# Performance work log

Measured on AMD Instinct MI355X. Metric: run time of the kernel, lower is better.

## Reference

```python
import jax, jax.numpy as jnp
import numpy as np
from jax import lax

V, E, H, D = 50000, 300, 128, 128   # vocab, embed, gru_units, dense_units
B, S, W, T = 32, 512, 20, 16        # batch, sentences/doc, words/sentence, topics/doc


def setup_inputs() -> dict:
    key = jax.random.key(0)
    ks = jax.random.split(key, 16)
    word_ids = jax.random.randint(ks[0], (B, S, W), 0, V, dtype=jnp.int32)
    # contiguous equal topic segments, 1-based inclusive boundaries
    L = S // T
    starts = (1 + np.arange(T) * L).astype(np.int32)
    ends = (starts + L - 1).astype(np.int32)
    topic_start_ends = jnp.asarray(np.broadcast_to(np.stack([starts, ends], -1), (B, T, 2)))
    sc = 0.05
    def rn(k, shape, s=sc):
        return jax.random.normal(k, shape, dtype=jnp.float32) * s
    inp = {
        "word_ids": word_ids,
        "topic_start_ends": topic_start_ends,
        "emb": rn(ks[1], (V, E), 0.6),
        "Wih_f": rn(ks[2], (3 * H, E)), "Whh_f": rn(ks[3], (3 * H, H)),
        "bih_f": rn(ks[4], (3 * H,)),   "bhh_f": rn(ks[5], (3 * H,)),
        "Wih_b": rn(ks[6], (3 * H, E)), "Whh_b": rn(ks[7], (3 * H, H)),
        "bih_b": rn(ks[8], (3 * H,)),   "bhh_b": rn(ks[9], (3 * H,)),
        "W_att": rn(ks[10], (4 * H, 4 * H)), "v_att": rn(ks[11], (4 * H, 1)),
        "W1": rn(ks[12], (D, 4 * H)), "b1": rn(ks[13], (D,)),
        "W2": rn(ks[14], (1, D)),     "b2": rn(ks[15], (1,)),
    }
    return inp


def _gru_dir(x_sbe, Wih, Whh, bih, bhh, reverse):
    """x_sbe: [S,B,E] -> (outputs [S,B,H] in original time order, last hidden [B,H])."""
    h0 = jnp.zeros((x_sbe.shape[1], Whh.shape[1]), x_sbe.dtype)
    def step(h, xt):
        gx = xt @ Wih.T + bih            # [B,3H]
        gh = h @ Whh.T + bhh
        xr, xz, xn = jnp.split(gx, 3, axis=-1)   # PyTorch gate order: r,z,n
        hr, hz, hn = jnp.split(gh, 3, axis=-1)
        r = jax.nn.sigmoid(xr + hr)
        z = jax.nn.sigmoid(xz + hz)
        n = jnp.tanh(xn + r * hn)
        h2 = (1.0 - z) * n + z * h
        return h2, h2
    last, outs = lax.scan(step, h0, x_sbe, reverse=reverse)
    return outs, last


def reference(word_ids, topic_start_ends, emb,
              Wih_f, Whh_f, bih_f, bhh_f,
              Wih_b, Whh_b, bih_b, bhh_b,
              W_att, v_att, W1, b1, W2, b2):
    # --- sent_encoder: mean word embedding per sentence ---
    x = jnp.mean(emb[word_ids], axis=2)              # [B,S,E]
    # --- doc_encoder: biGRU over sentences ---
    xs = jnp.swapaxes(x, 0, 1)                       # [S,B,E]
    out_f, last_f = _gru_dir(xs, Wih_f, Whh_f, bih_f, bhh_f, reverse=False)
    out_b, last_b = _gru_dir(xs, Wih_b, Whh_b, bih_b, bhh_b, reverse=True)
    sent_rep = jnp.swapaxes(jnp.concatenate([out_f, out_b], axis=-1), 0, 1)  # [B,S,2H]
    # faithful to torch hidden.view(B, 2H) on [2,B,H] contiguous memory
    doc_vec = jnp.stack([last_f, last_b], axis=0).reshape(sent_rep.shape[0], 2 * last_f.shape[1])
    doc_rep = jnp.broadcast_to(doc_vec[:, None, :], sent_rep.shape)          # [B,S,2H]
    # --- topic segment extraction via boundary diffs on zero-padded GRU out ---
    Bn, Sn, twoH = sent_rep.shape
    Hn = twoH // 2
    P = jnp.pad(sent_rep, ((0, 0), (1, 1), (0, 0)))   # [B,S+2,2H]; index i = 1-based sentence i
    starts = topic_start_ends[..., 0]                 # [B,T], 1-based
    ends = topic_start_ends[..., 1]
    bidx = jnp.arange(Bn)[:, None]
    fw = P[bidx, ends, :Hn] - P[bidx, starts - 1, :Hn]      # forward-dir diff
    bw = P[bidx, starts, Hn:] - P[bidx, ends + 1, Hn:]      # backward-dir diff
    topic_mat = jnp.concatenate([fw, bw], axis=-1)          # [B,T,2H]
    # scatter: sentence s (0-based) belongs to topic with starts-1 <= s <= ends-1
    pos = jnp.arange(Sn, dtype=starts.dtype) + 1            # 1-based sentence ids
    seg = jax.vmap(lambda st: jnp.searchsorted(st, pos, side='right') - 1)(starts)  # [B,S]
    topic_rep = jnp.take_along_axis(topic_mat, seg[..., None], axis=1)              # [B,S,2H]
    # --- decoder ---
    cat_ds = jnp.concatenate([doc_rep, sent_rep], axis=-1)   # [B,S,4H]
    cat_ts = jnp.concatenate([topic_rep, sent_rep], axis=-1)
    doc_scores = jnp.tanh(cat_ds @ W_att) @ v_att            # [B,S,1]
    topic_scores = jnp.tanh(cat_ts @ W_att) @ v_att
    ssum = doc_scores + topic_scores
    context = (doc_scores / ssum) * doc_rep + (topic_scores / ssum) * topic_rep
    inp = jnp.concatenate([sent_rep, context], axis=-1)      # [B,S,4H]
    h = jax.nn.relu(inp @ W1.T + b1)                         # dropout = identity (eval)
    logits = h @ W2.T + b2                                   # [B,S,1]
    return logits
```

## Files before the change

kernel.cpp:

```cpp
#include <hip/hip_runtime.h>
#include <hip/hip_bf16.h>

#define B_ 32
#define S_ 512
#define W_ 20
#define T_ 16
#define E_ 300
#define H_ 128
#define M_ (B_*S_)

#define OFF_GX        0ul
#define OFF_X         12582912ul
#define OFF_SENT      17498112ul
#define OFF_LASTF     21692416ul
#define OFF_LASTB     21696512ul
#define OFF_DOCVEC    21700608ul
#define OFF_TOPICMAT  21708800ul
#define OFF_DOCPART   21839872ul
#define OFF_TOPICPART 21856256ul
#define OFF_SEG       22118400ul
#define OFF_WTIH      22134784ul
#define OFF_BIASIH    22365184ul
#define OFF_W1T       22365952ul
#define OFF_H         22431488ul
#define OFF_SRPART    0ul
#define OFF_CTX       OFF_X

__global__ void prep_kernel(const float* __restrict__ Wih_f, const float* __restrict__ Wih_b,
                            const float* __restrict__ bih_f, const float* __restrict__ bih_b,
                            const float* __restrict__ W1,
                            float* __restrict__ Wt_ih, float* __restrict__ bias_ih,
                            float* __restrict__ W1t) {
  int idx = blockIdx.x * 256 + threadIdx.x;
  if (idx < E_ * 768) {
    int k = idx / 768, g = idx % 768;
    Wt_ih[idx] = (g < 384) ? Wih_f[g * E_ + k] : Wih_b[(g - 384) * E_ + k];
  }
  if (idx < 768) bias_ih[idx] = (idx < 384) ? bih_f[idx] : bih_b[idx - 384];
  if (idx < 512 * 128) { int k = idx / 128, j = idx % 128; W1t[idx] = W1[j * 512 + k]; }
}

__global__ void embed_mean_kernel(const int* __restrict__ wid, const float* __restrict__ emb,
                                  float* __restrict__ x) {
  int m = blockIdx.x;
  const int* ids = wid + (size_t)m * W_;
  int e = threadIdx.x;
  float s0 = 0.f, s1 = 0.f, s2 = 0.f;
  for (int w = 0; w < W_; w++) {
    const float* row = emb + (size_t)ids[w] * E_;
    s0 += row[e];
    s1 += row[e + 128];
    if (e < E_ - 256) s2 += row[e + 256];
  }
  const float inv = 1.0f / (float)W_;
  float* xr = x + (size_t)m * E_;
  xr[e] = s0 * inv; xr[e + 128] = s1 * inv; if (e < E_ - 256) xr[e + 256] = s2 * inv;
}

template<bool BIAS, bool ACCUM, bool RELU>
__global__ __launch_bounds__(256) void gemm64(
    const float* __restrict__ A, int lda,
    const float* __restrict__ B, int ldb,
    float* __restrict__ C, int ldc,
    const float* __restrict__ bias,
    int M, int N, int K) {
  __shared__ float As[16][68];
  __shared__ float Bs[16][68];
  const int tid = threadIdx.x;
  const int n0 = blockIdx.x * 64, m0 = blockIdx.y * 64;
  const int tx = tid & 15, ty = tid >> 4;
  const int am = tid >> 2, ak = (tid & 3) << 2;
  const int bk = tid >> 4, bn = (tid & 15) << 2;
  float acc[4][4] = {};
  for (int k0 = 0; k0 < K; k0 += 16) {
    float4 av = make_float4(0.f, 0.f, 0.f, 0.f);
    int arow = m0 + am;
    if (arow < M) {
      if (k0 + ak + 3 < K) {
        av = *(const float4*)(A + (size_t)arow * lda + k0 + ak);
      } else {
        float tmp[4] = {0.f, 0.f, 0.f, 0.f};
        #pragma unroll
        for (int i2 = 0; i2 < 4; i2++) { int k = k0 + ak + i2; if (k < K) tmp[i2] = A[(size_t)arow * lda + k]; }
        av = make_float4(tmp[0], tmp[1], tmp[2], tmp[3]);
      }
    }
    As[ak + 0][am] = av.x; As[ak + 1][am] = av.y; As[ak + 2][am] = av.z; As[ak + 3][am] = av.w;
    float4 bv = make_float4(0.f, 0.f, 0.f, 0.f);
    {
      int k = k0 + bk;
      if (k < K) bv = *(const float4*)(B + (size_t)k * ldb + n0 + bn);
    }
    *(float4*)&Bs[bk][bn] = bv;
    __syncthreads();
    #pragma unroll
    for (int kk = 0; kk < 16; kk++) {
      float4 a = *(const float4*)&As[kk][ty << 2];
      float4 b = *(const float4*)&Bs[kk][tx << 2];
      acc[0][0] = fmaf(a.x, b.x, acc[0][0]); acc[0][1] = fmaf(a.x, b.y, acc[0][1]);
      acc[0][2] = fmaf(a.x, b.z, acc[0][2]); acc[0][3] = fmaf(a.x, b.w, acc[0][3]);
      acc[1][0] = fmaf(a.y, b.x, acc[1][0]); acc[1][1] = fmaf(a.y, b.y, acc[1][1]);
      acc[1][2] = fmaf(a.y, b.z, acc[1][2]); acc[1][3] = fmaf(a.y, b.w, acc[1][3]);
      acc[2][0] = fmaf(a.z, b.x, acc[2][0]); acc[2][1] = fmaf(a.z, b.y, acc[2][1]);
      acc[2][2] = fmaf(a.z, b.z, acc[2][2]); acc[2][3] = fmaf(a.z, b.w, acc[2][3]);
      acc[3][0] = fmaf(a.w, b.x, acc[3][0]); acc[3][1] = fmaf(a.w, b.y, acc[3][1]);
      acc[3][2] = fmaf(a.w, b.z, acc[3][2]); acc[3][3] = fmaf(a.w, b.w, acc[3][3]);
    }
    __syncthreads();
  }
  float4 bias4 = make_float4(0.f, 0.f, 0.f, 0.f);
  if (BIAS) bias4 = *(const float4*)(bias + n0 + (tx << 2));
  #pragma unroll
  for (int i = 0; i < 4; i++) {
    int row = m0 + (ty << 2) + i;
    if (row >= M) break;
    float* cp = C + (size_t)row * ldc + n0 + (tx << 2);
    float4 v = make_float4(acc[i][0], acc[i][1], acc[i][2], acc[i][3]);
    if (BIAS) { v.x += bias4.x; v.y += bias4.y; v.z += bias4.z; v.w += bias4.w; }
    if (ACCUM) { float4 o = *(const float4*)cp; v.x += o.x; v.y += o.y; v.z += o.z; v.w += o.w; }
    if (RELU) { v.x = fmaxf(v.x, 0.f); v.y = fmaxf(v.y, 0.f); v.z = fmaxf(v.z, 0.f); v.w = fmaxf(v.w, 0.f); }
    *(float4*)cp = v;
  }
}

#define PIN4(v) asm volatile("" : "+v"((v).x), "+v"((v).y), "+v"((v).z), "+v"((v).w))
__global__ __launch_bounds__(512) __attribute__((amdgpu_waves_per_eu(2, 2)))
void gru_kernel(
    const float* __restrict__ gxbuf,
    const float* __restrict__ Whh_f, const float* __restrict__ Whh_b,
    const float* __restrict__ bhh_f, const float* __restrict__ bhh_b,
    float* __restrict__ sent_rep,
    float* __restrict__ last_f, float* __restrict__ last_b) {
  const int bid = blockIdx.x;
  const int dir = bid >> 5, b = bid & 31;
  const int t = threadIdx.x;
  const int wave = t >> 6;
  const int lane = t & 63;
  const int q = lane >> 4;
  const int j = (wave << 4) + (lane & 15);
  const int k0 = q << 5;
  const float* Whh = dir ? Whh_b : Whh_f;
  const float* bhh = dir ? bhh_b : bhh_f;

  float4 wr4[8], wz4[8], wn4[8];
  #pragma unroll
  for (int i = 0; i < 8; i++) {
    wr4[i] = *(const float4*)(Whh + (size_t)j * 128 + k0 + i * 4);
    wz4[i] = *(const float4*)(Whh + (size_t)(128 + j) * 128 + k0 + i * 4);
    wn4[i] = *(const float4*)(Whh + (size_t)(256 + j) * 128 + k0 + i * 4);
  }
  #pragma unroll
  for (int i = 0; i < 8; i++) { PIN4(wr4[i]); PIN4(wz4[i]); PIN4(wn4[i]); }

  const float bhr = bhh[j], bhz = bhh[128 + j], bhn = bhh[256 + j];
  const int gate = q ? (q - 1) : 2;
  const float mr = (q == 1) ? 1.f : 0.f;
  const float mz = (q == 2) ? 1.f : 0.f;
  const float* gxp = gxbuf + (size_t)b * 512 * 768 + dir * 384 + gate * 128 + j;

  __shared__ float hbuf[2][128];
  if (t < 128) hbuf[0][t] = 0.f;
  __syncthreads();

  float hprev = 0.f;
  int ts = dir ? 511 : 0;
  const int stp = dir ? -1 : 1;
  float* srow = sent_rep + (size_t)b * 512 * 256 + dir * 128;

  float gx_c = gxp[(size_t)ts * 768];
  float gx_1 = gxp[(size_t)(ts + stp) * 768];

  #pragma unroll 1
  for (int s = 0; s < 512; s++) {
    float gx_2 = 0.f;
    if (s + 2 < 512) gx_2 = gxp[(size_t)(ts + 2 * stp) * 768];
    const float4* h4 = (const float4*)(&hbuf[s & 1][k0]);
    float pr = 0.f, pz = 0.f, pn = 0.f;
    #pragma unroll
    for (int i = 0; i < 8; i++) {
      float4 hv = h4[i];
      pr = fmaf(wr4[i].x, hv.x, pr); pr = fmaf(wr4[i].y, hv.y, pr);
      pr = fmaf(wr4[i].z, hv.z, pr); pr = fmaf(wr4[i].w, hv.w, pr);
      pz = fmaf(wz4[i].x, hv.x, pz); pz = fmaf(wz4[i].y, hv.y, pz);
      pz = fmaf(wz4[i].z, hv.z, pz); pz = fmaf(wz4[i].w, hv.w, pz);
      pn = fmaf(wn4[i].x, hv.x, pn); pn = fmaf(wn4[i].y, hv.y, pn);
      pn = fmaf(wn4[i].z, hv.z, pn); pn = fmaf(wn4[i].w, hv.w, pn);
    }
    pr = fmaf(mr, gx_c, pr);
    pz = fmaf(mz, gx_c, pz);
    pr += __shfl_xor(pr, 16); pr += __shfl_xor(pr, 32);
    pz += __shfl_xor(pz, 16); pz += __shfl_xor(pz, 32);
    pn += __shfl_xor(pn, 16); pn += __shfl_xor(pn, 32);
    float gn = __shfl(gx_c, (lane & 15) + 48);
    float r = 1.f / (1.f + expf(-(pr + bhr)));
    float z = 1.f / (1.f + expf(-(pz + bhz)));
    float n = tanhf(gn + r * (pn + bhn));
    float hnew = (1.f - z) * n + z * hprev;
    hprev = hnew;
    if (q == 0) {
      hbuf[(s + 1) & 1][j] = hnew;
      srow[(size_t)ts * 256 + j] = hnew;
    }
    __syncthreads();
    ts += stp;
    gx_c = gx_1; gx_1 = gx_2;
  }
  if (q == 0) (dir ? last_b : last_f)[b * 128 + j] = hprev;
}

__global__ void docvec_kernel(const float* __restrict__ last_f, const float* __restrict__ last_b,
                              float* __restrict__ doc_vec) {
  int idx = blockIdx.x * 256 + threadIdx.x;
  int i = idx >> 8, c = idx & 255;
  const float* src = (i < 16) ? last_f : last_b;
  int ii = (i < 16) ? i : i - 16;
  int bb = 2 * ii + (c >> 7);
  doc_vec[idx] = src[bb * 128 + (c & 127)];
}

__global__ void topicmat_kernel(const float* __restrict__ sent_rep, const int* __restrict__ tse,
                                float* __restrict__ topic_mat) {
  int bt = blockIdx.x;
  int b = bt >> 4, t = bt & 15;
  int st = tse[(b * 16 + t) * 2 + 0];
  int en = tse[(b * 16 + t) * 2 + 1];
  int jj = threadIdx.x;
  const float* sr = sent_rep + (size_t)b * 512 * 256;
  float val;
  if (jj < 128) {
    float a = sr[(size_t)(en - 1) * 256 + jj];
    float c = (st - 2 >= 0) ? sr[(size_t)(st - 2) * 256 + jj] : 0.f;
    val = a - c;
  } else {
    float a = sr[(size_t)(st - 1) * 256 + jj];
    float c = (en <= 511) ? sr[(size_t)en * 256 + jj] : 0.f;
    val = a - c;
  }
  topic_mat[(size_t)bt * 256 + jj] = val;
}

__global__ void seg_kernel(const int* __restrict__ tse, int* __restrict__ seg) {
  int idx = blockIdx.x * 256 + threadIdx.x;
  int b = idx >> 9, s = idx & 511;
  int pos = s + 1, cnt = 0;
  for (int t = 0; t < T_; t++) cnt += (tse[(b * T_ + t) * 2] <= pos);
  int sg = cnt - 1; sg = sg < 0 ? 0 : (sg > T_ - 1 ? T_ - 1 : sg);
  seg[idx] = sg;
}

__global__ void scores_ctx_kernel(const float* __restrict__ sr_part,
                                  const float* __restrict__ doc_part,
                                  const float* __restrict__ topic_part,
                                  const float* __restrict__ v_att,
                                  const float* __restrict__ doc_vec,
                                  const float* __restrict__ topic_mat,
                                  const int* __restrict__ seg,
                                  float* __restrict__ context) {
  int wid = threadIdx.x >> 6, lane = threadIdx.x & 63;
  int row = blockIdx.x * 4 + wid;
  int b = row >> 9;
  int sg = seg[row];
  const float* srp = sr_part + (size_t)row * 512;
  const float* dp = doc_part + (size_t)b * 512;
  const float* tp = topic_part + (size_t)(b * 16 + sg) * 512;
  float accd = 0.f, acct = 0.f;
  #pragma unroll
  for (int i = 0; i < 8; i++) {
    int n = lane + i * 64;
    float sp = srp[n], va = v_att[n];
    accd += tanhf(dp[n] + sp) * va;
    acct += tanhf(tp[n] + sp) * va;
  }
  #pragma unroll
  for (int off = 32; off; off >>= 1) { accd += __shfl_xor(accd, off); acct += __shfl_xor(acct, off); }
  float ssum = accd + acct;
  float rd = accd / ssum, rt = acct / ssum;
  const float* dv = doc_vec + (size_t)b * 256;
  const float* tm = topic_mat + (size_t)(b * 16 + sg) * 256;
  float* ctx = context + (size_t)row * 256;
  #pragma unroll
  for (int i = 0; i < 4; i++) {
    int jj = lane + i * 64;
    ctx[jj] = rd * dv[jj] + rt * tm[jj];
  }
}

__global__ void logits_kernel(const float* __restrict__ h, const float* __restrict__ W2,
                              const float* __restrict__ b2, float* __restrict__ out, int M) {
  int wid = threadIdx.x >> 6, lane = threadIdx.x & 63;
  int row = blockIdx.x * 4 + wid;
  if (row >= M) return;
  const float* hp = h + (size_t)row * 128;
  float s = hp[lane] * W2[lane] + hp[lane + 64] * W2[lane + 64];
  #pragma unroll
  for (int off = 32; off; off >>= 1) s += __shfl_xor(s, off);
  if (lane == 0) out[row] = s + b2[0];
}

extern "C" void kernel_launch(void* const* d_in, const int* in_sizes, int n_in,
                              void* d_out, int out_size, void* d_ws, size_t ws_size,
                              hipStream_t stream) {
  const int*   word_ids = (const int*)d_in[0];
  const int*   tse      = (const int*)d_in[1];
  const float* emb      = (const float*)d_in[2];
  const float* Wih_f    = (const float*)d_in[3];
  const float* Whh_f    = (const float*)d_in[4];
  const float* bih_f    = (const float*)d_in[5];
  const float* bhh_f    = (const float*)d_in[6];
  const float* Wih_b    = (const float*)d_in[7];
  const float* Whh_b    = (const float*)d_in[8];
  const float* bih_b    = (const float*)d_in[9];
  const float* bhh_b    = (const float*)d_in[10];
  const float* W_att    = (const float*)d_in[11];
  const float* v_att    = (const float*)d_in[12];
  const float* W1       = (const float*)d_in[13];
  const float* b1       = (const float*)d_in[14];
  const float* W2       = (const float*)d_in[15];
  const float* b2       = (const float*)d_in[16];
  float* ws  = (float*)d_ws;
  float* out = (float*)d_out;

  prep_kernel<<<900, 256, 0, stream>>>(Wih_f, Wih_b, bih_f, bih_b, W1,
                                       ws + OFF_WTIH, ws + OFF_BIASIH, ws + OFF_W1T);
  embed_mean_kernel<<<M_, 128, 0, stream>>>(word_ids, emb, ws + OFF_X);
  gemm64<true, false, false><<<dim3(12, 256), 256, 0, stream>>>(
      ws + OFF_X, E_, ws + OFF_WTIH, 768, ws + OFF_GX, 768, ws + OFF_BIASIH, M_, 768, E_);
  gru_kernel<<<64, 512, 0, stream>>>(ws + OFF_GX, Whh_f, Whh_b, bhh_f, bhh_b,
                                     ws + OFF_SENT, ws + OFF_LASTF, ws + OFF_LASTB);
  docvec_kernel<<<32, 256, 0, stream>>>(ws + OFF_LASTF, ws + OFF_LASTB, ws + OFF_DOCVEC);
  topicmat_kernel<<<512, 256, 0, stream>>>(ws + OFF_SENT, tse, ws + OFF_TOPICMAT);
  seg_kernel<<<64, 256, 0, stream>>>(tse, (int*)(ws + OFF_SEG));
  gemm64<false, false, false><<<dim3(8, 1), 256, 0, stream>>>(
      ws + OFF_DOCVEC, 256, W_att, 512, ws + OFF_DOCPART, 512, nullptr, 32, 512, 256);
  gemm64<false, false, false><<<dim3(8, 8), 256, 0, stream>>>(
      ws + OFF_TOPICMAT, 256, W_att, 512, ws + OFF_TOPICPART, 512, nullptr, 512, 512, 256);
  gemm64<false, false, false><<<dim3(8, 256), 256, 0, stream>>>(
      ws + OFF_SENT, 256, W_att + 256 * 512, 512, ws + OFF_SRPART, 512, nullptr, M_, 512, 256);
  scores_ctx_kernel<<<M_ / 4, 256, 0, stream>>>(
      ws + OFF_SRPART, ws + OFF_DOCPART, ws + OFF_TOPICPART, v_att,
      ws + OFF_DOCVEC, ws + OFF_TOPICMAT, (const int*)(ws + OFF_SEG), ws + OFF_CTX);
  gemm64<true, false, false><<<dim3(2, 256), 256, 0, stream>>>(
      ws + OFF_SENT, 256, ws + OFF_W1T, 128, ws + OFF_H, 128, b1, M_, 128, 256);
  gemm64<false, true, true><<<dim3(2, 256), 256, 0, stream>>>(
      ws + OFF_CTX, 256, ws + OFF_W1T + 256 * 128, 128, ws + OFF_H, 128, nullptr, M_, 128, 256);
  logits_kernel<<<M_ / 4, 256, 0, stream>>>(ws + OFF_H, W2, b2, out, M_);
}
```

Baseline: 733.7 us.

## Hold GRU recurrent weights in AGPRs and remap lanes for cheap reductions

Restructures the sequential GRU recurrence kernel. The 96 weight values per thread move into accumulation registers via inline assembly and are read back with v_accvgpr_read during hand-written FMA chains, which frees architectural VGPRs. Lanes are remapped so the four k-partials for an output are adjacent, turning the cross-lane reductions into xor-1/2 shuffles. The hidden-state LDS buffer is swizzled, bias handling is folded into the accumulator init, and expf/tanhf are replaced by clamped __expf formulas. The loop is also unrolled by two, at the cost of fragile inline asm and slightly reduced precision in the activations.

```diff
diff --git a/kernel.cpp b/kernel.cpp
--- a/kernel.cpp
+++ b/kernel.cpp
@@ -8,6 +8,8 @@
 #define E_ 300
 #define H_ 128
 #define M_ (B_*S_)
+
+typedef float f32x4 __attribute__((ext_vector_type(4)));
 
 #define OFF_GX        0ul
 #define OFF_X         12582912ul
@@ -123,9 +125,25 @@
   }
 }
 
-#define PIN4(v) asm volatile("" : "+v"((v).x), "+v"((v).y), "+v"((v).z), "+v"((v).w))
-__global__ __launch_bounds__(512) __attribute__((amdgpu_waves_per_eu(2, 2)))
-void gru_kernel(
+#define SWZ(k) ((k) + 4 * ((k) >> 4))
+
+#define AW(N, V) asm volatile("v_accvgpr_write_b32 a" #N ", %0" :: "v"(V) : "a" #N)
+#define AWQ(N0, N1, N2, N3, Q) do { AW(N0, (Q).x); AW(N1, (Q).y); AW(N2, (Q).z); AW(N3, (Q).w); } while (0)
+
+#define A96CLOB \
+  "a0","a1","a2","a3","a4","a5","a6","a7","a8","a9","a10","a11","a12","a13","a14","a15", \
+  "a16","a17","a18","a19","a20","a21","a22","a23","a24","a25","a26","a27","a28","a29","a30","a31", \
+  "a32","a33","a34","a35","a36","a37","a38","a39","a40","a41","a42","a43","a44","a45","a46","a47", \
+  "a48","a49","a50","a51","a52","a53","a54","a55","a56","a57","a58","a59","a60","a61","a62","a63", \
+  "a64","a65","a66","a67","a68","a69","a70","a71","a72","a73","a74","a75","a76","a77","a78","a79", \
+  "a80","a81","a82","a83","a84","a85","a86","a87","a88","a89","a90","a91","a92","a93","a94","a95"
+
+#define RD(T, N) "v_accvgpr_read_b32 %[" #T "], a" #N "\n\t"
+#define FM(P, T, X) "v_fmac_f32 %[" #P "], %[" #T "], %[" #X "]\n\t"
+#define COLA(CR, CZ, CN, X) \
+  RD(t0, CR) RD(t1, CZ) RD(t2, CN) FM(pr, t0, X) FM(pz, t1, X) FM(pn, t2, X)
+
+__global__ __launch_bounds__(512, 2) void gru_kernel(
     const float* __restrict__ gxbuf,
     const float* __restrict__ Whh_f, const float* __restrict__ Whh_b,
     const float* __restrict__ bhh_f, const float* __restrict__ bhh_b,
@@ -134,77 +152,119 @@
   const int bid = blockIdx.x;
   const int dir = bid >> 5, b = bid & 31;
   const int t = threadIdx.x;
-  const int wave = t >> 6;
-  const int lane = t & 63;
-  const int q = lane >> 4;
-  const int j = (wave << 4) + (lane & 15);
+  const int j = t >> 2;
+  const int q = t & 3;
   const int k0 = q << 5;
   const float* Whh = dir ? Whh_b : Whh_f;
   const float* bhh = dir ? bhh_b : bhh_f;
 
-  float4 wr4[8], wz4[8], wn4[8];
-  #pragma unroll
-  for (int i = 0; i < 8; i++) {
-    wr4[i] = *(const float4*)(Whh + (size_t)j * 128 + k0 + i * 4);
-    wz4[i] = *(const float4*)(Whh + (size_t)(128 + j) * 128 + k0 + i * 4);
-    wn4[i] = *(const float4*)(Whh + (size_t)(256 + j) * 128 + k0 + i * 4);
-  }
-  #pragma unroll
-  for (int i = 0; i < 8; i++) { PIN4(wr4[i]); PIN4(wz4[i]); PIN4(wn4[i]); }
-
-  const float bhr = bhh[j], bhz = bhh[128 + j], bhn = bhh[256 + j];
-  const int gate = q ? (q - 1) : 2;
+  {
+    const float* Wr = Whh + (size_t)j * 128 + k0;
+    const float* Wz = Whh + (size_t)(128 + j) * 128 + k0;
+    const float* Wn = Whh + (size_t)(256 + j) * 128 + k0;
+    f32x4 w0 = *(const f32x4*)(Wr + 0),  w1 = *(const f32x4*)(Wr + 4);
+    f32x4 w2 = *(const f32x4*)(Wr + 8),  w3 = *(const f32x4*)(Wr + 12);
+    f32x4 w4 = *(const f32x4*)(Wr + 16), w5 = *(const f32x4*)(Wr + 20);
+    f32x4 w6 = *(const f32x4*)(Wr + 24), w7 = *(const f32x4*)(Wr + 28);
+    AWQ(0, 1, 2, 3, w0);   AWQ(4, 5, 6, 7, w1);   AWQ(8, 9, 10, 11, w2);  AWQ(12, 13, 14, 15, w3);
+    AWQ(16, 17, 18, 19, w4); AWQ(20, 21, 22, 23, w5); AWQ(24, 25, 26, 27, w6); AWQ(28, 29, 30, 31, w7);
+    w0 = *(const f32x4*)(Wz + 0);  w1 = *(const f32x4*)(Wz + 4);
+    w2 = *(const f32x4*)(Wz + 8);  w3 = *(const f32x4*)(Wz + 12);
+    w4 = *(const f32x4*)(Wz + 16); w5 = *(const f32x4*)(Wz + 20);
+    w6 = *(const f32x4*)(Wz + 24); w7 = *(const f32x4*)(Wz + 28);
+    AWQ(32, 33, 34, 35, w0); AWQ(36, 37, 38, 39, w1); AWQ(40, 41, 42, 43, w2); AWQ(44, 45, 46, 47, w3);
+    AWQ(48, 49, 50, 51, w4); AWQ(52, 53, 54, 55, w5); AWQ(56, 57, 58, 59, w6); AWQ(60, 61, 62, 63, w7);
+    w0 = *(const f32x4*)(Wn + 0);  w1 = *(const f32x4*)(Wn + 4);
+    w2 = *(const f32x4*)(Wn + 8);  w3 = *(const f32x4*)(Wn + 12);
+    w4 = *(const f32x4*)(Wn + 16); w5 = *(const f32x4*)(Wn + 20);
+    w6 = *(const f32x4*)(Wn + 24); w7 = *(const f32x4*)(Wn + 28);
+    AWQ(64, 65, 66, 67, w0); AWQ(68, 69, 70, 71, w1); AWQ(72, 73, 74, 75, w2); AWQ(76, 77, 78, 79, w3);
+    AWQ(80, 81, 82, 83, w4); AWQ(84, 85, 86, 87, w5); AWQ(88, 89, 90, 91, w6); AWQ(92, 93, 94, 95, w7);
+  }
+
+  const float cR = (q == 0) ? bhh[j] : 0.f;
+  const float cZ = (q == 0) ? bhh[128 + j] : 0.f;
+  const float cN = (q == 0) ? bhh[256 + j] : 0.f;
+  const int gate = (q == 1) ? 0 : (q == 2) ? 1 : 2;
   const float mr = (q == 1) ? 1.f : 0.f;
   const float mz = (q == 2) ? 1.f : 0.f;
-  const float* gxp = gxbuf + (size_t)b * 512 * 768 + dir * 384 + gate * 128 + j;
-
-  __shared__ float hbuf[2][128];
-  if (t < 128) hbuf[0][t] = 0.f;
+
+  __shared__ float lds[320];
+  if (t < 128) lds[SWZ(t)] = 0.f;
   __syncthreads();
 
+  const int stp = dir ? -1 : 1;
+  const int ts0 = dir ? 511 : 0;
+  const ptrdiff_t g768 = (ptrdiff_t)stp * 768;
+  const ptrdiff_t s256 = (ptrdiff_t)stp * 256;
+  const float* gq = gxbuf + (size_t)b * 512 * 768 + dir * 384 + gate * 128 + j + (size_t)ts0 * 768;
+  float* sp = sent_rep + (size_t)b * 512 * 256 + dir * 128 + (size_t)ts0 * 256;
   float hprev = 0.f;
-  int ts = dir ? 511 : 0;
-  const int stp = dir ? -1 : 1;
-  float* srow = sent_rep + (size_t)b * 512 * 256 + dir * 128;
-
-  float gx_c = gxp[(size_t)ts * 768];
-  float gx_1 = gxp[(size_t)(ts + stp) * 768];
+  float gx_c = gq[0];
+  float gx_1 = gq[g768];
+
+#define GRU_STEP(P, SOFF) do { \
+    float gx_2 = 0.f; \
+    if (s + 2 + (SOFF) < 512) gx_2 = gq[2 * g768]; \
+    const f32x4* hv = (const f32x4*)(lds + (P) * 160 + 40 * q); \
+    f32x4 h0 = hv[0], h1 = hv[1], h2 = hv[2], h3 = hv[3]; \
+    f32x4 h4 = hv[5], h5 = hv[6], h6 = hv[7], h7 = hv[8]; \
+    float pr = cR, pz = cZ, pn = cN; \
+    { float t0v, t1v, t2v; \
+      asm volatile( \
+        COLA(0,32,64,x0)   COLA(1,33,65,x1)   COLA(2,34,66,x2)   COLA(3,35,67,x3) \
+        COLA(4,36,68,x4)   COLA(5,37,69,x5)   COLA(6,38,70,x6)   COLA(7,39,71,x7) \
+        COLA(8,40,72,x8)   COLA(9,41,73,x9)   COLA(10,42,74,x10) COLA(11,43,75,x11) \
+        COLA(12,44,76,x12) COLA(13,45,77,x13) COLA(14,46,78,x14) COLA(15,47,79,x15) \
+        : [pr]"+v"(pr), [pz]"+v"(pz), [pn]"+v"(pn), \
+          [t0]"=&v"(t0v), [t1]"=&v"(t1v), [t2]"=&v"(t2v) \
+        : [x0]"v"(h0.x), [x1]"v"(h0.y), [x2]"v"(h0.z), [x3]"v"(h0.w), \
+          [x4]"v"(h1.x), [x5]"v"(h1.y), [x6]"v"(h1.z), [x7]"v"(h1.w), \
+          [x8]"v"(h2.x), [x9]"v"(h2.y), [x10]"v"(h2.z), [x11]"v"(h2.w), \
+          [x12]"v"(h3.x), [x13]"v"(h3.y), [x14]"v"(h3.z), [x15]"v"(h3.w) \
+        : A96CLOB); \
+      asm volatile( \
+        COLA(16,48,80,x0)  COLA(17,49,81,x1)  COLA(18,50,82,x2)  COLA(19,51,83,x3) \
+        COLA(20,52,84,x4)  COLA(21,53,85,x5)  COLA(22,54,86,x6)  COLA(23,55,87,x7) \
+        COLA(24,56,88,x8)  COLA(25,57,89,x9)  COLA(26,58,90,x10) COLA(27,59,91,x11) \
+        COLA(28,60,92,x12) COLA(29,61,93,x13) COLA(30,62,94,x14) COLA(31,63,95,x15) \
+        : [pr]"+v"(pr), [pz]"+v"(pz), [pn]"+v"(pn), \
+          [t0]"=&v"(t0v), [t1]"=&v"(t1v), [t2]"=&v"(t2v) \
+        : [x0]"v"(h4.x), [x1]"v"(h4.y), [x2]"v"(h4.z), [x3]"v"(h4.w), \
+          [x4]"v"(h5.x), [x5]"v"(h5.y), [x6]"v"(h5.z), [x7]"v"(h5.w), \
+          [x8]"v"(h6.x), [x9]"v"(h6.y), [x10]"v"(h6.z), [x11]"v"(h6.w), \
+          [x12]"v"(h7.x), [x13]"v"(h7.y), [x14]"v"(h7.z), [x15]"v"(h7.w) \
+        : A96CLOB); } \
+    pr = fmaf(mr, gx_c, pr); \
+    pz = fmaf(mz, gx_c, pz); \
+    pr += __shfl_xor(pr, 1); pr += __shfl_xor(pr, 2); \
+    pz += __shfl_xor(pz, 1); pz += __shfl_xor(pz, 2); \
+    pn += __shfl_xor(pn, 1); pn += __shfl_xor(pn, 2); \
+    float xr = fminf(fmaxf(pr, -30.f), 30.f); \
+    float xz = fminf(fmaxf(pz, -30.f), 30.f); \
+    float r = 1.f / (1.f + __expf(-xr)); \
+    float z = 1.f / (1.f + __expf(-xz)); \
+    float xn = gx_c + r * pn; xn = fminf(fmaxf(xn, -15.f), 15.f); \
+    float e2 = __expf(2.f * xn); \
+    float n = (e2 - 1.f) / (e2 + 1.f); \
+    float hnew = (1.f - z) * n + z * hprev; \
+    hprev = hnew; \
+    if (q == 0) { \
+      lds[((P) ^ 1) * 160 + SWZ(j)] = hnew; \
+      sp[j] = hnew; \
+    } \
+    __syncthreads(); \
+    gq += g768; sp += s256; \
+    gx_c = gx_1; gx_1 = gx_2; \
+  } while (0)
 
   #pragma unroll 1
-  for (int s = 0; s < 512; s++) {
-    float gx_2 = 0.f;
-    if (s + 2 < 512) gx_2 = gxp[(size_t)(ts + 2 * stp) * 768];
-    const float4* h4 = (const float4*)(&hbuf[s & 1][k0]);
-    float pr = 0.f, pz = 0.f, pn = 0.f;
-    #pragma unroll
-    for (int i = 0; i < 8; i++) {
-      float4 hv = h4[i];
-      pr = fmaf(wr4[i].x, hv.x, pr); pr = fmaf(wr4[i].y, hv.y, pr);
-      pr = fmaf(wr4[i].z, hv.z, pr); pr = fmaf(wr4[i].w, hv.w, pr);
-      pz = fmaf(wz4[i].x, hv.x, pz); pz = fmaf(wz4[i].y, hv.y, pz);
-      pz = fmaf(wz4[i].z, hv.z, pz); pz = fmaf(wz4[i].w, hv.w, pz);
-      pn = fmaf(wn4[i].x, hv.x, pn); pn = fmaf(wn4[i].y, hv.y, pn);
-      pn = fmaf(wn4[i].z, hv.z, pn); pn = fmaf(wn4[i].w, hv.w, pn);
-    }
-    pr = fmaf(mr, gx_c, pr);
-    pz = fmaf(mz, gx_c, pz);
-    pr += __shfl_xor(pr, 16); pr += __shfl_xor(pr, 32);
-    pz += __shfl_xor(pz, 16); pz += __shfl_xor(pz, 32);
-    pn += __shfl_xor(pn, 16); pn += __shfl_xor(pn, 32);
-    float gn = __shfl(gx_c, (lane & 15) + 48);
-    float r = 1.f / (1.f + expf(-(pr + bhr)));
-    float z = 1.f / (1.f + expf(-(pz + bhz)));
-    float n = tanhf(gn + r * (pn + bhn));
-    float hnew = (1.f - z) * n + z * hprev;
-    hprev = hnew;
-    if (q == 0) {
-      hbuf[(s + 1) & 1][j] = hnew;
-      srow[(size_t)ts * 256 + j] = hnew;
-    }
-    __syncthreads();
-    ts += stp;
-    gx_c = gx_1; gx_1 = gx_2;
-  }
+  for (int s = 0; s < 512; s += 2) {
+    GRU_STEP(0, 0);
+    GRU_STEP(1, 1);
+  }
+#undef GRU_STEP
+
   if (q == 0) (dir ? last_b : last_f)[b * 128 + j] = hprev;
 }
 
```

After: 771.1 us. 1.05x slower.
